# Kernel tuning notes

Measured on AMD Instinct MI355X. Metric: run time of the kernel, lower is better.

Reference implementation:

```python
import jax, jax.numpy as jnp
import numpy as np

N = 100000      # nodes
E = 1600000     # edges (avg degree 16)
D_IN = 64
D_OUT = 64
EPS = 1e-9


def setup_inputs() -> dict:
    key = jax.random.key(0)
    ks = jax.random.split(key, 12)
    x = jax.random.normal(ks[0], (N, D_IN), dtype=jnp.float32)
    edge_row = jax.random.randint(ks[1], (E,), 0, N, dtype=jnp.int32)
    edge_col = jax.random.randint(ks[2], (E,), 0, N, dtype=jnp.int32)
    # positive normalized adjacency values (~1/degree scale)
    edge_val = jax.random.uniform(ks[3], (E,), dtype=jnp.float32) / 16.0
    lim = float(np.sqrt(6.0 / (D_IN + D_OUT)))  # xavier_uniform
    W0 = jax.random.uniform(ks[4], (D_OUT, D_IN), jnp.float32, -lim, lim)
    W1 = jax.random.uniform(ks[5], (D_OUT, D_IN), jnp.float32, -lim, lim)
    b0 = jnp.zeros((D_OUT,), jnp.float32)
    b1 = jnp.zeros((D_OUT,), jnp.float32)
    scale0 = jnp.ones((D_OUT,), jnp.float32)
    scale1 = jnp.ones((D_OUT,), jnp.float32)
    offset0 = jnp.zeros((D_OUT,), jnp.float32)
    offset1 = jnp.zeros((D_OUT,), jnp.float32)
    return {"x": x, "edge_val": edge_val, "W0": W0, "b0": b0,
            "scale0": scale0, "offset0": offset0, "W1": W1, "b1": b1,
            "scale1": scale1, "offset1": offset1,
            "edge_row": edge_row, "edge_col": edge_col}


def _hop_transform(feat, W, b, scale, offset):
    # Linear (no bias in nn.Linear) + separate bias + ReLU
    h = jax.nn.relu(feat @ W.T + b)                      # [N, D_OUT]
    # custom per-row normalization ('norm' branch)
    mean = jnp.mean(h, axis=1, keepdims=True)
    var = jnp.var(h, axis=1, keepdims=True) + EPS        # unbiased=False
    return (h - mean) * scale * jax.lax.rsqrt(var) + offset


def reference(x, edge_val, W0, b0, scale0, offset0, W1, b1, scale1, offset1,
              edge_row, edge_col):
    # SpMM: out[r] = sum_{e: row[e]==r} val[e] * x[col[e]]
    msgs = edge_val[:, None] * x[edge_col]               # [E, D_IN]
    agg = jax.ops.segment_sum(msgs, edge_row, num_segments=N)
    # order=1: hop-0 uses raw features, hop-1 uses aggregated features
    h0 = _hop_transform(x, W0, b0, scale0, offset0)
    h1 = _hop_transform(agg, W1, b1, scale1, offset1)
    # aggr='mean' -> elementwise sum of partial features
    return h0 + h1
```

## Files before the change

### kernel.cpp

```cpp
#include <hip/hip_runtime.h>

#define NN 100000
#define NE 1600000
#define DD 64
#define NB   391
#define NBK1 391
#define BCAP 4608
#define RCAP 40
#define NK3  1563

__device__ __forceinline__ unsigned short f2bfu(float f) {
    union { float f; unsigned u; } c; c.f = f;
    unsigned lsb = (c.u >> 16) & 1u;
    c.u += 0x7FFFu + lsb;
    return (unsigned short)(c.u >> 16);
}

typedef short v8s __attribute__((ext_vector_type(8)));
typedef float v4f __attribute__((ext_vector_type(4)));

__global__ __launch_bounds__(256) void prep_kernel(
    const float* __restrict__ x, const float* __restrict__ W0,
    const float* __restrict__ W1, unsigned short* __restrict__ xb,
    int* __restrict__ gbcur,
    unsigned short* __restrict__ wb0, unsigned short* __restrict__ wb1)
{
    int t = threadIdx.x, blk = blockIdx.x;
    if (blk < 16) {
        int j = blk * 256 + t;
        if (j < NB) gbcur[j] = 0;
        if (j < DD * DD) { wb0[j] = f2bfu(W0[j]); wb1[j] = f2bfu(W1[j]); }
    }
    int i = (blk * 256 + t) * 8;
    float4 a = *(const float4*)(x + i);
    float4 b = *(const float4*)(x + i + 4);
    uint4 o;
    o.x = (unsigned)f2bfu(a.x) | ((unsigned)f2bfu(a.y) << 16);
    o.y = (unsigned)f2bfu(a.z) | ((unsigned)f2bfu(a.w) << 16);
    o.z = (unsigned)f2bfu(b.x) | ((unsigned)f2bfu(b.y) << 16);
    o.w = (unsigned)f2bfu(b.z) | ((unsigned)f2bfu(b.w) << 16);
    *(uint4*)(xb + i) = o;
}

__global__ __launch_bounds__(512) void bin_scatter_kernel(
    const int* __restrict__ row, const int* __restrict__ col,
    const float* __restrict__ val, int* __restrict__ gbcur,
    int2* __restrict__ bslab)
{
    __shared__ int2 rbuf[4096];
    __shared__ unsigned short bkts[4096];
    __shared__ int pscan[512];
    __shared__ int cnt[NB];
    __shared__ int pst[NB];
    __shared__ int cur[NB];
    __shared__ int gbase[NB];

    int b = blockIdx.x, t = threadIdx.x;
    int e0 = b * 4096;

    for (int i = t; i < NB; i += 512) cnt[i] = 0;
    __syncthreads();

    int4 r[2], c[2]; float4 v[2]; bool ok[2];
#pragma unroll
    for (int h = 0; h < 2; ++h) {
        int e = e0 + t * 8 + h * 4;
        ok[h] = (e + 3 < NE);
        if (ok[h]) {
            r[h] = *(const int4*)(row + e);
            c[h] = *(const int4*)(col + e);
            v[h] = *(const float4*)(val + e);
            atomicAdd(&cnt[r[h].x >> 8], 1);
            atomicAdd(&cnt[r[h].y >> 8], 1);
            atomicAdd(&cnt[r[h].z >> 8], 1);
            atomicAdd(&cnt[r[h].w >> 8], 1);
        }
    }
    __syncthreads();
    pscan[t] = (t < NB) ? cnt[t] : 0;
    __syncthreads();
    for (int off = 1; off < 512; off <<= 1) {
        int u = (t >= off) ? pscan[t - off] : 0;
        __syncthreads();
        pscan[t] += u;
        __syncthreads();
    }
    if (t < NB) {
        int st = pscan[t] - cnt[t];
        pst[t] = st;
        cur[t] = st;
        gbase[t] = cnt[t] ? atomicAdd(&gbcur[t], cnt[t]) : 0;
    }
    __syncthreads();
#pragma unroll
    for (int h = 0; h < 2; ++h) {
        if (ok[h]) {
            int bk, pos;
            bk = r[h].x >> 8; pos = atomicAdd(&cur[bk], 1);
            rbuf[pos] = make_int2(c[h].x | ((r[h].x & 255) << 17), __float_as_int(v[h].x));
            bkts[pos] = (unsigned short)bk;
            bk = r[h].y >> 8; pos = atomicAdd(&cur[bk], 1);
            rbuf[pos] = make_int2(c[h].y | ((r[h].y & 255) << 17), __float_as_int(v[h].y));
            bkts[pos] = (unsigned short)bk;
            bk = r[h].z >> 8; pos = atomicAdd(&cur[bk], 1);
            rbuf[pos] = make_int2(c[h].z | ((r[h].z & 255) << 17), __float_as_int(v[h].z));
            bkts[pos] = (unsigned short)bk;
            bk = r[h].w >> 8; pos = atomicAdd(&cur[bk], 1);
            rbuf[pos] = make_int2(c[h].w | ((r[h].w & 255) << 17), __float_as_int(v[h].w));
            bkts[pos] = (unsigned short)bk;
        }
    }
    __syncthreads();
    int ntot = pscan[511];
    for (int i = t; i < ntot; i += 512) {
        int bk = bkts[i];
        int gi = gbase[bk] + (i - pst[bk]);
        if (gi < BCAP) bslab[(size_t)bk * BCAP + gi] = rbuf[i];
    }
}

#define BF4FMA(G, VV, ACC) { \
    ACC.x = fmaf(VV, __uint_as_float((G).x << 16), ACC.x); \
    ACC.y = fmaf(VV, __uint_as_float((G).x & 0xFFFF0000u), ACC.y); \
    ACC.z = fmaf(VV, __uint_as_float((G).y << 16), ACC.z); \
    ACC.w = fmaf(VV, __uint_as_float((G).y & 0xFFFF0000u), ACC.w); }

__global__ __launch_bounds__(256, 7) void sort_pull_mfma_kernel(
    const unsigned short* __restrict__ xb, const int* __restrict__ gbcur,
    const int2* __restrict__ bslab,
    const unsigned short* __restrict__ wb0, const unsigned short* __restrict__ wb1,
    const float* __restrict__ b0, const float* __restrict__ s0, const float* __restrict__ o0,
    const float* __restrict__ b1, const float* __restrict__ s1, const float* __restrict__ o1,
    float* __restrict__ out)
{
    __shared__ int2 ebuf[64][RCAP];
    __shared__ int cur[64];

    int phys = blockIdx.x;
    int xc = phys & 7, ii = phys >> 3;
    int p = (xc < 3) ? xc * 196 + ii : 588 + (xc - 3) * 195 + ii;

    int t = threadIdx.x, lane = t & 63, wv = t >> 6;
    int sub = lane & 15, q = lane >> 4;
    int bkt = p >> 2, quarter = p & 3;
    int nb = min(gbcur[bkt], BCAP);
    const int2* bp = bslab + (size_t)bkt * BCAP;

    if (t < 64) cur[t] = 0;
    __syncthreads();
    for (int i = t; i < nb; i += 256) {
        int2 rc = bp[i];
        int rl = (rc.x >> 17) & 255;
        if ((rl >> 6) == quarter) {
            int pos = atomicAdd(&cur[rl & 63], 1);
            if (pos < RCAP) ebuf[rl & 63][pos] = make_int2(rc.x & 0x1FFFF, rc.y);
        }
    }
    __syncthreads();

    int nb0 = p * 64 + wv * 16;
    if (nb0 < NN) {
        for (int rr = 0; rr < 16; ++rr) {
            int lr = wv * 16 + rr;
            int d = min(cur[lr], RCAP);
            int cc = (d + 7) >> 3;
            int plen = cc * 8;
            if (lane < plen - d) ebuf[lr][d + lane] = make_int2(0, 0);

            float4 acc = make_float4(0.f, 0.f, 0.f, 0.f);
            int ch = 0;
            for (; ch + 2 <= cc; ch += 2) {
                int2 r0 = ebuf[lr][ch * 8 + q];
                int2 r1 = ebuf[lr][ch * 8 + 4 + q];
                int2 r2 = ebuf[lr][ch * 8 + 8 + q];
                int2 r3 = ebuf[lr][ch * 8 + 12 + q];
                uint2 g0 = *(const uint2*)(xb + (size_t)r0.x * DD + sub * 4);
                uint2 g1 = *(const uint2*)(xb + (size_t)r1.x * DD + sub * 4);
                uint2 g2 = *(const uint2*)(xb + (size_t)r2.x * DD + sub * 4);
                uint2 g3 = *(const uint2*)(xb + (size_t)r3.x * DD + sub * 4);
                float v0 = __int_as_float(r0.y), v1 = __int_as_float(r1.y);
                float v2 = __int_as_float(r2.y), v3 = __int_as_float(r3.y);
                BF4FMA(g0, v0, acc); BF4FMA(g1, v1, acc);
                BF4FMA(g2, v2, acc); BF4FMA(g3, v3, acc);
            }
            if (ch < cc) {
                int2 r0 = ebuf[lr][ch * 8 + q];
                int2 r1 = ebuf[lr][ch * 8 + 4 + q];
                uint2 g0 = *(const uint2*)(xb + (size_t)r0.x * DD + sub * 4);
                uint2 g1 = *(const uint2*)(xb + (size_t)r1.x * DD + sub * 4);
                float v0 = __int_as_float(r0.y), v1 = __int_as_float(r1.y);
                BF4FMA(g0, v0, acc); BF4FMA(g1, v1, acc);
            }
            acc.x += __shfl_xor(acc.x, 16, 64); acc.y += __shfl_xor(acc.y, 16, 64);
            acc.z += __shfl_xor(acc.z, 16, 64); acc.w += __shfl_xor(acc.w, 16, 64);
            acc.x += __shfl_xor(acc.x, 32, 64); acc.y += __shfl_xor(acc.y, 32, 64);
            acc.z += __shfl_xor(acc.z, 32, 64); acc.w += __shfl_xor(acc.w, 32, 64);
            if (q == 0) {
                uint2 pk;
                pk.x = (unsigned)f2bfu(acc.x) | ((unsigned)f2bfu(acc.y) << 16);
                pk.y = (unsigned)f2bfu(acc.z) | ((unsigned)f2bfu(acc.w) << 16);
                *(uint2*)&(((unsigned*)&ebuf[lr][0])[sub * 2]) = pk;
            }
        }

        v8s ax[2], aa[2];
#pragma unroll
        for (int ks = 0; ks < 2; ++ks) {
            ax[ks] = *(const v8s*)(xb + (size_t)(nb0 + sub) * DD + ks * 32 + q * 8);
            aa[ks] = *(const v8s*)&(((unsigned*)&ebuf[wv * 16 + sub][0])[ks * 16 + q * 4]);
        }

        float h0v[4][4], h1v[4][4];
        float sr0[4] = {0,0,0,0}, sq0[4] = {0,0,0,0};
        float sr1[4] = {0,0,0,0}, sq1[4] = {0,0,0,0};
#pragma unroll
        for (int dt = 0; dt < 4; ++dt) {
            int nidx = dt * 16 + sub;
            float bi0 = b0[nidx], bi1 = b1[nidx];
            v8s w00 = *(const v8s*)(wb0 + nidx * 64 + q * 8);
            v8s w01 = *(const v8s*)(wb0 + nidx * 64 + 32 + q * 8);
            v8s w10 = *(const v8s*)(wb1 + nidx * 64 + q * 8);
            v8s w11 = *(const v8s*)(wb1 + nidx * 64 + 32 + q * 8);
            v4f c0 = (v4f){bi0, bi0, bi0, bi0};
            v4f c1 = (v4f){bi1, bi1, bi1, bi1};
            c0 = __builtin_amdgcn_mfma_f32_16x16x32_bf16(ax[0], w00, c0, 0, 0, 0);
            c0 = __builtin_amdgcn_mfma_f32_16x16x32_bf16(ax[1], w01, c0, 0, 0, 0);
            c1 = __builtin_amdgcn_mfma_f32_16x16x32_bf16(aa[0], w10, c1, 0, 0, 0);
            c1 = __builtin_amdgcn_mfma_f32_16x16x32_bf16(aa[1], w11, c1, 0, 0, 0);
#pragma unroll
            for (int r = 0; r < 4; ++r) {
                float h = fmaxf(c0[r], 0.f); h0v[dt][r] = h; sr0[r] += h; sq0[r] += h * h;
                float g = fmaxf(c1[r], 0.f); h1v[dt][r] = g; sr1[r] += g; sq1[r] += g * g;
            }
        }
#pragma unroll
        for (int off = 1; off < 16; off <<= 1) {
#pragma unroll
            for (int r = 0; r < 4; ++r) {
                sr0[r] += __shfl_xor(sr0[r], off, 64);
                sq0[r] += __shfl_xor(sq0[r], off, 64);
                sr1[r] += __shfl_xor(sr1[r], off, 64);
                sq1[r] += __shfl_xor(sq1[r], off, 64);
            }
        }

        float scl0[4], scl1[4], ofs0[4], ofs1[4];
#pragma unroll
        for (int dt = 0; dt < 4; ++dt) {
            int nidx = dt * 16 + sub;
            scl0[dt] = s0[nidx]; scl1[dt] = s1[nidx];
            ofs0[dt] = o0[nidx]; ofs1[dt] = o1[nidx];
        }

        const float inv = 1.0f / 64.0f;
#pragma unroll
        for (int r = 0; r < 4; ++r) {
            float m0 = sr0[r] * inv;
            float v0 = fmaxf(sq0[r] * inv - m0 * m0, 0.f) + 1e-9f;
            float m1 = sr1[r] * inv;
            float v1 = fmaxf(sq1[r] * inv - m1 * m1, 0.f) + 1e-9f;
            float rs0 = rsqrtf(v0), rs1 = rsqrtf(v1);
            int node = nb0 + q * 4 + r;
#pragma unroll
            for (int dt = 0; dt < 4; ++dt) {
                float rv = (h0v[dt][r] - m0) * scl0[dt] * rs0 + ofs0[dt]
                         + (h1v[dt][r] - m1) * scl1[dt] * rs1 + ofs1[dt];
                out[(size_t)node * DD + dt * 16 + sub] = rv;
            }
        }
    }
}

extern "C" void kernel_launch(void* const* d_in, const int* in_sizes, int n_in,
                              void* d_out, int out_size, void* d_ws, size_t ws_size,
                              hipStream_t stream) {
    const float* x  = (const float*)d_in[0];
    const float* ev = (const float*)d_in[1];
    const float* W0 = (const float*)d_in[2];
    const float* b0 = (const float*)d_in[3];
    const float* s0 = (const float*)d_in[4];
    const float* o0 = (const float*)d_in[5];
    const float* W1 = (const float*)d_in[6];
    const float* b1 = (const float*)d_in[7];
    const float* s1 = (const float*)d_in[8];
    const float* o1 = (const float*)d_in[9];
    const int* row = (const int*)d_in[10];
    const int* col = (const int*)d_in[11];

    char* wsb = (char*)d_ws;
    int*  gbcur = (int*)wsb;
    unsigned short* wb0 = (unsigned short*)(wsb + 1600);
    unsigned short* wb1 = (unsigned short*)(wsb + 9792);
    unsigned short* xb = (unsigned short*)(wsb + 18048);
    int2* bslab = (int2*)(wsb + 12818048);

    prep_kernel<<<3125, 256, 0, stream>>>(x, W0, W1, xb, gbcur, wb0, wb1);
    bin_scatter_kernel<<<NBK1, 512, 0, stream>>>(row, col, ev, gbcur, bslab);
    sort_pull_mfma_kernel<<<NK3, 256, 0, stream>>>(
        xb, gbcur, bslab, wb0, wb1, b0, s0, o0, b1, s1, o1, (float*)d_out);
}
```

Baseline: 175.0 us.

## Fuse bf16 prep into bin-scatter kernel and use wave-shuffle prefix scan

The separate x/W bf16 conversion kernel is merged into the edge binning kernel: each of the 391 blocks converts a strided slice of x before it bins its edges, and block 0 also converts the weights. The gbcur counter reset moves to a hipMemsetAsync. The 512-wide shared-memory Hillis-Steele scan, which needed many barriers, is replaced by a wavefront shuffle scan plus a per-wave total combine. This removes one kernel launch and many syncthreads, at the cost of extra serial work per block before binning and an added memset call.

```diff
diff --git a/kernel.cpp b/kernel.cpp
--- a/kernel.cpp
+++ b/kernel.cpp
@@ -8,6 +8,7 @@
 #define BCAP 4608
 #define RCAP 40
 #define NK3  1563
+#define NXI  800000
 
 __device__ __forceinline__ unsigned short f2bfu(float f) {
     union { float f; unsigned u; } c; c.f = f;
@@ -19,48 +20,51 @@
 typedef short v8s __attribute__((ext_vector_type(8)));
 typedef float v4f __attribute__((ext_vector_type(4)));
 
-__global__ __launch_bounds__(256) void prep_kernel(
-    const float* __restrict__ x, const float* __restrict__ W0,
-    const float* __restrict__ W1, unsigned short* __restrict__ xb,
-    int* __restrict__ gbcur,
+__global__ __launch_bounds__(512) void prep_bin_scatter_kernel(
+    const float* __restrict__ x, const int* __restrict__ row,
+    const int* __restrict__ col, const float* __restrict__ val,
+    const float* __restrict__ W0, const float* __restrict__ W1,
+    int* __restrict__ gbcur, int2* __restrict__ bslab,
+    unsigned short* __restrict__ xb,
     unsigned short* __restrict__ wb0, unsigned short* __restrict__ wb1)
-{
-    int t = threadIdx.x, blk = blockIdx.x;
-    if (blk < 16) {
-        int j = blk * 256 + t;
-        if (j < NB) gbcur[j] = 0;
-        if (j < DD * DD) { wb0[j] = f2bfu(W0[j]); wb1[j] = f2bfu(W1[j]); }
-    }
-    int i = (blk * 256 + t) * 8;
-    float4 a = *(const float4*)(x + i);
-    float4 b = *(const float4*)(x + i + 4);
-    uint4 o;
-    o.x = (unsigned)f2bfu(a.x) | ((unsigned)f2bfu(a.y) << 16);
-    o.y = (unsigned)f2bfu(a.z) | ((unsigned)f2bfu(a.w) << 16);
-    o.z = (unsigned)f2bfu(b.x) | ((unsigned)f2bfu(b.y) << 16);
-    o.w = (unsigned)f2bfu(b.z) | ((unsigned)f2bfu(b.w) << 16);
-    *(uint4*)(xb + i) = o;
-}
-
-__global__ __launch_bounds__(512) void bin_scatter_kernel(
-    const int* __restrict__ row, const int* __restrict__ col,
-    const float* __restrict__ val, int* __restrict__ gbcur,
-    int2* __restrict__ bslab)
 {
     __shared__ int2 rbuf[4096];
     __shared__ unsigned short bkts[4096];
-    __shared__ int pscan[512];
     __shared__ int cnt[NB];
     __shared__ int pst[NB];
     __shared__ int cur[NB];
     __shared__ int gbase[NB];
+    __shared__ int wtot[8];
+    __shared__ int sh_ntot;
 
     int b = blockIdx.x, t = threadIdx.x;
+    int lane = t & 63, wv = t >> 6;
+
+    for (int i = t; i < NB; i += 512) cnt[i] = 0;
+
+#pragma unroll
+    for (int k = 0; k < 4; ++k) {
+        int idx = b * 512 + t + k * (NBK1 * 512);
+        if (idx < NXI) {
+            const float* px = x + (size_t)idx * 8;
+            float4 a = *(const float4*)px;
+            float4 bb = *(const float4*)(px + 4);
+            uint4 o;
+            o.x = (unsigned)f2bfu(a.x) | ((unsigned)f2bfu(a.y) << 16);
+            o.y = (unsigned)f2bfu(a.z) | ((unsigned)f2bfu(a.w) << 16);
+            o.z = (unsigned)f2bfu(bb.x) | ((unsigned)f2bfu(bb.y) << 16);
+            o.w = (unsigned)f2bfu(bb.z) | ((unsigned)f2bfu(bb.w) << 16);
+            *(uint4*)(xb + (size_t)idx * 8) = o;
+        }
+    }
+    if (b == 0) {
+        for (int j = t; j < DD * DD; j += 512) {
+            wb0[j] = f2bfu(W0[j]); wb1[j] = f2bfu(W1[j]);
+        }
+    }
+    __syncthreads();
+
     int e0 = b * 4096;
-
-    for (int i = t; i < NB; i += 512) cnt[i] = 0;
-    __syncthreads();
-
     int4 r[2], c[2]; float4 v[2]; bool ok[2];
 #pragma unroll
     for (int h = 0; h < 2; ++h) {
@@ -77,21 +81,29 @@
         }
     }
     __syncthreads();
-    pscan[t] = (t < NB) ? cnt[t] : 0;
-    __syncthreads();
-    for (int off = 1; off < 512; off <<= 1) {
-        int u = (t >= off) ? pscan[t - off] : 0;
-        __syncthreads();
-        pscan[t] += u;
-        __syncthreads();
-    }
+
+    int vcnt = (t < NB) ? cnt[t] : 0;
+    int sv = vcnt;
+#pragma unroll
+    for (int off = 1; off < 64; off <<= 1) {
+        int u = __shfl_up(sv, off, 64);
+        if (lane >= off) sv += u;
+    }
+    if (lane == 63) wtot[wv] = sv;
+    __syncthreads();
+    int pre = 0;
+#pragma unroll
+    for (int w = 0; w < 8; ++w) pre += (w < wv) ? wtot[w] : 0;
+    int incl = sv + pre;
+    if (t == 511) sh_ntot = incl;
     if (t < NB) {
-        int st = pscan[t] - cnt[t];
+        int st = incl - vcnt;
         pst[t] = st;
         cur[t] = st;
-        gbase[t] = cnt[t] ? atomicAdd(&gbcur[t], cnt[t]) : 0;
-    }
-    __syncthreads();
+        gbase[t] = vcnt ? atomicAdd(&gbcur[t], vcnt) : 0;
+    }
+    __syncthreads();
+
 #pragma unroll
     for (int h = 0; h < 2; ++h) {
         if (ok[h]) {
@@ -111,7 +123,8 @@
         }
     }
     __syncthreads();
-    int ntot = pscan[511];
+
+    int ntot = sh_ntot;
     for (int i = t; i < ntot; i += 512) {
         int bk = bkts[i];
         int gi = gbase[bk] + (i - pst[bk]);
@@ -294,8 +307,9 @@
     unsigned short* xb = (unsigned short*)(wsb + 18048);
     int2* bslab = (int2*)(wsb + 12818048);
 
-    prep_kernel<<<3125, 256, 0, stream>>>(x, W0, W1, xb, gbcur, wb0, wb1);
-    bin_scatter_kernel<<<NBK1, 512, 0, stream>>>(row, col, ev, gbcur, bslab);
+    hipMemsetAsync(gbcur, 0, NB * sizeof(int), stream);
+    prep_bin_scatter_kernel<<<NBK1, 512, 0, stream>>>(
+        x, row, col, ev, W0, W1, gbcur, bslab, xb, wb0, wb1);
     sort_pull_mfma_kernel<<<NK3, 256, 0, stream>>>(
         xb, gbcur, bslab, wb0, wb1, b0, s0, o0, b1, s1, o1, (float*)d_out);
 }
```

Result: no change. 173.4 us (-0.9%).
